# Kernel optimization log

Measured on AMD Instinct MI355X. Metric: run time of the kernel, lower is better.

## Reference

```python
import jax, jax.numpy as jnp
import numpy as np

NG, CPN, K = 16, 24, 5          # ngroups, channels-per-group, kernel size
C = NG * CPN                     # 384 total channels
PAD = K // 2                     # PseudoEntropyPad(2, ...)


def build_mask():
    """PixelCNN-style group-causal mask for MaskConv2 (hidden/type-B: center
    position allows input group <= output group)."""
    m = np.zeros((C, C, K, K), np.float32)
    m[:, :, :PAD, :] = 1.0                      # rows above center: all allowed
    m[:, :, PAD, :PAD] = 1.0                    # center row, left of center
    g = np.arange(C) // CPN
    m[:, :, PAD, PAD] = (g[None, :] <= g[:, None]).astype(np.float32)
    return jnp.asarray(m)


def masked_conv(x, w, b, mask):
    # zero pad by 2 (PseudoEntropyPad) + VALID 5x5 conv == SAME conv
    y = jax.lax.conv_general_dilated(
        x, w * mask, window_strides=(1, 1), padding=[(PAD, PAD), (PAD, PAD)],
        dimension_numbers=("NCHW", "OIHW", "NCHW"))
    return y + b[None, :, None, None]


def prelu(x, a):
    return jnp.where(x >= 0, x, a[None, :, None, None] * x)


def setup_inputs() -> dict:
    key = jax.random.key(0)
    ks = jax.random.split(key, 5)
    x = jax.random.normal(ks[0], (2, C, 256, 512), dtype=jnp.float32)
    w1 = jax.random.normal(ks[1], (C, C, K, K), dtype=jnp.float32) * 0.02
    w2 = jax.random.normal(ks[2], (C, C, K, K), dtype=jnp.float32) * 0.02
    b1 = jnp.zeros((C,), jnp.float32)
    b2 = jnp.zeros((C,), jnp.float32)
    a1 = jnp.full((C,), 0.25, jnp.float32)   # PReLU init
    a2 = jnp.full((C,), 0.25, jnp.float32)
    return {"x": x, "w1": w1, "b1": b1, "a1": a1, "w2": w2, "b2": b2, "a2": a2}


def reference(x, w1, b1, a1, w2, b2, a2):
    mask = build_mask()
    y = prelu(masked_conv(x, w1, b1, mask), a1)   # EntropyConv 1 (pad+conv+PReLU+trim)
    y = prelu(masked_conv(y, w2, b2, mask), a2)   # EntropyConv 2
    return y + x                                   # residual
```

## Files before the change

### kernel.cpp

```cpp
#include <hip/hip_runtime.h>
#include <hip/hip_bf16.h>


#define C_CH 384
#define HH   256
#define WWD  512
#define NN   2
#define NC   12
#define PR   260
#define PC   516
#define ICS  (PR * PC * 32)
#define TCOLS 144
#define TSHORTS (4 * TCOLS * 32)

typedef __attribute__((ext_vector_type(8))) short short8;
typedef __attribute__((ext_vector_type(4))) float f32x4;

typedef const __attribute__((address_space(1))) void* gas_t;
typedef __attribute__((address_space(3))) void* las_t;

__device__ inline unsigned short f2bf(float f) {
    union { float f; unsigned int u; } v; v.f = f;
    unsigned int r = v.u + 0x7FFFu + ((v.u >> 16) & 1u);
    return (unsigned short)(r >> 16);
}

__global__ __launch_bounds__(256) void k_prepack(const float* __restrict__ w1, const float* __restrict__ w2,
                                                 unsigned short* __restrict__ wp1, unsigned short* __restrict__ wp2) {
    int idx = blockIdx.x * 256 + threadIdx.x;
    const int TOT = 13 * NC * C_CH * 32;
    if (idx >= TOT) return;
    int iq = idx & 31;
    int o  = (idx >> 5) % C_CH;
    int ic = (idx / (32 * C_CH)) % NC;
    int t  = idx / (32 * C_CH * NC);
    int i  = ic * 32 + iq;
    int kh = t < 5 ? 0 : (t < 10 ? 1 : 2);
    int kw = t < 5 ? t : (t < 10 ? t - 5 : t - 10);
    bool keep = (t != 12) || ((i / 24) <= (o / 24));
    int src = ((o * C_CH + i) * 5 + kh) * 5 + kw;
    wp1[idx] = keep ? f2bf(w1[src]) : (unsigned short)0;
    wp2[idx] = keep ? f2bf(w2[src]) : (unsigned short)0;
}

__global__ __launch_bounds__(256) void k_repack_x(const float* __restrict__ x, unsigned short* __restrict__ xc) {
    int bid = blockIdx.x;
    int w0 = (bid & 7) << 6;
    int h  = (bid >> 3) & 255;
    int n  = bid >> 11;
    int wi = threadIdx.x & 63;
    int cq = threadIdx.x >> 6;
    int w  = w0 + wi;
    int inb = n * C_CH * HH * WWD + h * WWD + w;
    for (int cc = 0; cc < NC; ++cc) {
        int c0 = cc * 32 + cq * 8;
        short8 outv;
        #pragma unroll
        for (int k = 0; k < 8; ++k) {
            float f = x[inb + (c0 + k) * (HH * WWD)];
            outv[k] = (short)f2bf(f);
        }
        int oidx = (n * NC + cc) * ICS + (h + 2) * (PC * 32) + (w + 2) * 32 + cq * 8;
        *(short8*)&xc[oidx] = outv;
    }
}

template<int SECOND>
__global__ __launch_bounds__(256, 2) void k_conv(const unsigned short* __restrict__ in,
                                                 const unsigned short* __restrict__ wp,
                                                 const float* __restrict__ bias,
                                                 const float* __restrict__ alpha,
                                                 const float* __restrict__ xres,
                                                 void* __restrict__ outp) {
    __shared__ __align__(16) unsigned short Xs[2][TSHORTS];

    int bid0 = blockIdx.x;
    int xcd = bid0 & 7;
    int j0  = bid0 >> 3;
    int tile = xcd * 128 + j0 / 3;
    int ob   = j0 % 3;
    int n    = tile >> 9;
    int hp   = (tile >> 2) & 127;
    int wseg = tile & 3;
    int w0 = wseg << 7, o0 = ob << 7, h0 = hp << 1;

    int tid = threadIdx.x;
    int lane = tid & 63;
    int wv = tid >> 6;
    int wr = wv >> 1, wc = wv & 1;
    int lg = lane >> 4, lm = lane & 15;

    int goff[9];
    #pragma unroll
    for (int it = 0; it < 9; ++it) {
        int k = wv * 9 + it;
        int s = k * 64 + lane;
        int r = s / 576;
        int rem = s - r * 576;
        int c = rem >> 2, q = rem & 3;
        int ce = c < 132 ? c : 0;
        goff[it] = ((h0 + r) * PC + (w0 + ce)) * 32 + q * 8;
    }

    f32x4 acc[32];
    #pragma unroll
    for (int i = 0; i < 32; ++i) acc[i] = (f32x4){0.f, 0.f, 0.f, 0.f};

    {
        const unsigned short* gbase = in + (n * NC + 0) * ICS;
        #pragma unroll
        for (int it = 0; it < 9; ++it) {
            const unsigned short* gp = gbase + goff[it];
            unsigned short* lp = &Xs[0][(wv * 9 + it) * 512];
            __builtin_amdgcn_global_load_lds((gas_t)gp, (las_t)lp, 16, 0, 0);
        }
    }
    __syncthreads();

    for (int ic = 0; ic < NC; ++ic) {
        int buf = ic & 1;
        const unsigned short* gnext = in + (n * NC + (ic + 1)) * ICS;
        short8 wb[4], wbn[4];
        {
            const unsigned short* wb0 = wp + ((0 * NC + ic) * C_CH + o0 + wc * 64) * 32;
            #pragma unroll
            for (int j = 0; j < 4; ++j) wb[j] = *(const short8*)&wb0[(j * 16 + lm) * 32 + lg * 8];
        }
        #pragma unroll
        for (int t = 0; t < 13; ++t) {
            if (t < 12) {
                const unsigned short* wbp = wp + (((t + 1) * NC + ic) * C_CH + o0 + wc * 64) * 32;
                #pragma unroll
                for (int j = 0; j < 4; ++j) wbn[j] = *(const short8*)&wbp[(j * 16 + lm) * 32 + lg * 8];
            }
            if (t < 9) {
                if (ic < NC - 1) {
                    const unsigned short* gp = gnext + goff[t];
                    unsigned short* lp = &Xs[buf ^ 1][(wv * 9 + t) * 512];
                    __builtin_amdgcn_global_load_lds((gas_t)gp, (las_t)lp, 16, 0, 0);
                }
            }
            int kh = t < 5 ? 0 : (t < 10 ? 1 : 2);
            int kw = t < 5 ? t : (t < 10 ? t - 5 : t - 10);
            short8 xa[8];
            #pragma unroll
            for (int f = 0; f < 8; ++f) {
                int cx = f * 16 + lm + kw;
                xa[f] = *(const short8*)&Xs[buf][(wr + kh) * (TCOLS * 32) + cx * 32 + lg * 8];
            }
            if (SECOND) {
                #pragma unroll
                for (int i = 0; i < 4; ++i)
                    #pragma unroll
                    for (int j = 0; j < 8; ++j)
                        acc[i * 8 + j] = __builtin_amdgcn_mfma_f32_16x16x32_bf16(wb[i], xa[j], acc[i * 8 + j], 0, 0, 0);
            } else {
                #pragma unroll
                for (int f = 0; f < 8; ++f)
                    #pragma unroll
                    for (int j = 0; j < 4; ++j)
                        acc[f * 4 + j] = __builtin_amdgcn_mfma_f32_16x16x32_bf16(xa[f], wb[j], acc[f * 4 + j], 0, 0, 0);
            }
            if (t < 12) {
                #pragma unroll
                for (int j = 0; j < 4; ++j) wb[j] = wbn[j];
            }
        }
        __syncthreads();
    }

    int h = h0 + wr;
    if (!SECOND) {
        unsigned short* y = (unsigned short*)outp;
        #pragma unroll
        for (int j = 0; j < 4; ++j) {
            int o = o0 + wc * 64 + j * 16 + lm;
            float bo = bias[o], ao = alpha[o];
            int base = (n * NC + (o >> 5)) * ICS + (h + 2) * (PC * 32) + (o & 31);
            #pragma unroll
            for (int f = 0; f < 8; ++f) {
                #pragma unroll
                for (int rr = 0; rr < 4; ++rr) {
                    int p = f * 16 + lg * 4 + rr;
                    float v = acc[f * 4 + j][rr] + bo;
                    v = v >= 0.f ? v : ao * v;
                    y[base + (w0 + p + 2) * 32] = f2bf(v);
                }
            }
        }
    } else {
        float* outf = (float*)outp;
        #pragma unroll
        for (int i = 0; i < 4; ++i) {
            #pragma unroll
            for (int rr = 0; rr < 4; ++rr) {
                int o = o0 + wc * 64 + i * 16 + lg * 4 + rr;
                float bo = bias[o], ao = alpha[o];
                #pragma unroll
                for (int j = 0; j < 8; ++j) {
                    int w = w0 + j * 16 + lm;
                    float v = acc[i * 8 + j][rr] + bo;
                    v = v >= 0.f ? v : ao * v;
                    int idx = ((n * C_CH + o) * HH + h) * WWD + w;
                    outf[idx] = v + xres[idx];
                }
            }
        }
    }
}

extern "C" void kernel_launch(void* const* d_in, const int* in_sizes, int n_in,
                              void* d_out, int out_size, void* d_ws, size_t ws_size,
                              hipStream_t stream) {
    const float* x  = (const float*)d_in[0];
    const float* w1 = (const float*)d_in[1];
    const float* b1 = (const float*)d_in[2];
    const float* a1 = (const float*)d_in[3];
    const float* w2 = (const float*)d_in[4];
    const float* b2 = (const float*)d_in[5];
    const float* a2 = (const float*)d_in[6];

    const size_t PLANE_SHORTS = (size_t)NN * NC * ICS;
    unsigned short* xc  = (unsigned short*)d_out;
    unsigned short* yb  = (unsigned short*)d_ws;
    unsigned short* wp1 = yb + PLANE_SHORTS;
    unsigned short* wp2 = wp1 + 13 * NC * C_CH * 32;

    hipMemsetAsync(xc, 0, PLANE_SHORTS * 2, stream);
    hipMemsetAsync(yb, 0, PLANE_SHORTS * 2, stream);

    k_prepack<<<(13 * NC * C_CH * 32 + 255) / 256, 256, 0, stream>>>(w1, w2, wp1, wp2);
    k_repack_x<<<NN * HH * (WWD / 64), 256, 0, stream>>>(x, xc);
    k_conv<0><<<3072, 256, 0, stream>>>(xc, wp1, b1, a1, nullptr, (void*)yb);
    k_conv<1><<<3072, 256, 0, stream>>>(yb, wp2, b2, a2, x, (void*)d_out);
}
```

Measured before the change: 2.011 ms.

## Switch conv MFMA to 32x32x16 bf16 with 16-channel planar layout

Repacks activations and weights into 16-channel chunks and replaces 16x16x32 MFMAs with 32x32x16 MFMAs, each wave computing a 128-pixel by 64-output tile as 4x2 32x32 accumulators. The inner loop is software-pipelined, with weight fragments triple-buffered and LDS activation fragments double-buffered, and s_setprio raises priority around the MFMA bursts. The aim is fewer LDS reads per MFMA and better matrix-core utilization. The risks are higher register pressure under the 2-blocks-per-CU launch bound and more global weight loads per step.

```diff
diff --git a/kernel.cpp b/kernel.cpp
--- a/kernel.cpp
+++ b/kernel.cpp
@@ -6,15 +6,17 @@
 #define HH   256
 #define WWD  512
 #define NN   2
-#define NC   12
+#define NKC  24
 #define PR   260
 #define PC   516
-#define ICS  (PR * PC * 32)
+#define ICS16 (PR * PC * 16)
 #define TCOLS 144
-#define TSHORTS (4 * TCOLS * 32)
-
-typedef __attribute__((ext_vector_type(8))) short short8;
-typedef __attribute__((ext_vector_type(4))) float f32x4;
+#define PLANE_SH (4 * TCOLS * 16)
+#define TSH (2 * PLANE_SH)
+
+typedef __attribute__((ext_vector_type(8)))  short short8;
+typedef __attribute__((ext_vector_type(16))) float f32x16;
+typedef __attribute__((ext_vector_type(4)))  int   int4v;
 
 typedef const __attribute__((address_space(1))) void* gas_t;
 typedef __attribute__((address_space(3))) void* las_t;
@@ -28,13 +30,13 @@
 __global__ __launch_bounds__(256) void k_prepack(const float* __restrict__ w1, const float* __restrict__ w2,
                                                  unsigned short* __restrict__ wp1, unsigned short* __restrict__ wp2) {
     int idx = blockIdx.x * 256 + threadIdx.x;
-    const int TOT = 13 * NC * C_CH * 32;
+    const int TOT = 13 * NKC * C_CH * 16;
     if (idx >= TOT) return;
-    int iq = idx & 31;
-    int o  = (idx >> 5) % C_CH;
-    int ic = (idx / (32 * C_CH)) % NC;
-    int t  = idx / (32 * C_CH * NC);
-    int i  = ic * 32 + iq;
+    int iq = idx & 15;
+    int o  = (idx >> 4) % C_CH;
+    int kc = (idx / (16 * C_CH)) % NKC;
+    int t  = idx / (16 * C_CH * NKC);
+    int i  = kc * 16 + iq;
     int kh = t < 5 ? 0 : (t < 10 ? 1 : 2);
     int kw = t < 5 ? t : (t < 10 ? t - 5 : t - 10);
     bool keep = (t != 12) || ((i / 24) <= (o / 24));
@@ -52,7 +54,7 @@
     int cq = threadIdx.x >> 6;
     int w  = w0 + wi;
     int inb = n * C_CH * HH * WWD + h * WWD + w;
-    for (int cc = 0; cc < NC; ++cc) {
+    for (int cc = 0; cc < 12; ++cc) {
         int c0 = cc * 32 + cq * 8;
         short8 outv;
         #pragma unroll
@@ -60,7 +62,8 @@
             float f = x[inb + (c0 + k) * (HH * WWD)];
             outv[k] = (short)f2bf(f);
         }
-        int oidx = (n * NC + cc) * ICS + (h + 2) * (PC * 32) + (w + 2) * 32 + cq * 8;
+        int kc = cc * 2 + (cq >> 1);
+        int oidx = (n * NKC + kc) * ICS16 + ((h + 2) * PC + (w + 2)) * 16 + (cq & 1) * 8;
         *(short8*)&xc[oidx] = outv;
     }
 }
@@ -72,7 +75,7 @@
                                                  const float* __restrict__ alpha,
                                                  const float* __restrict__ xres,
                                                  void* __restrict__ outp) {
-    __shared__ __align__(16) unsigned short Xs[2][TSHORTS];
+    __shared__ __align__(16) unsigned short Xs[2][TSH];
 
     int bid0 = blockIdx.x;
     int xcd = bid0 & 7;
@@ -88,120 +91,136 @@
     int lane = tid & 63;
     int wv = tid >> 6;
     int wr = wv >> 1, wc = wv & 1;
-    int lg = lane >> 4, lm = lane & 15;
+    int lo5 = lane & 31, hi = lane >> 5;
 
     int goff[9];
     #pragma unroll
     for (int it = 0; it < 9; ++it) {
         int k = wv * 9 + it;
-        int s = k * 64 + lane;
-        int r = s / 576;
-        int rem = s - r * 576;
-        int c = rem >> 2, q = rem & 3;
-        int ce = c < 132 ? c : 0;
-        goff[it] = ((h0 + r) * PC + (w0 + ce)) * 32 + q * 8;
-    }
-
-    f32x4 acc[32];
+        int plane = k / 18;
+        int s = (k % 18) * 64 + lane;
+        int r = s / 288;
+        int rem = s - r * 288;
+        int col = rem >> 1, h16 = rem & 1;
+        goff[it] = plane * ICS16 + ((h0 + r) * PC + (w0 + col)) * 16 + h16 * 8;
+    }
+
+    const int KH[13] = {0,0,0,0,0,1,1,1,1,1,2,2,2};
+    const int KW[13] = {0,1,2,3,4,0,1,2,3,4,0,1,2};
+
+    f32x16 acc[4][2];
     #pragma unroll
-    for (int i = 0; i < 32; ++i) acc[i] = (f32x4){0.f, 0.f, 0.f, 0.f};
-
-    {
-        const unsigned short* gbase = in + (n * NC + 0) * ICS;
-        #pragma unroll
-        for (int it = 0; it < 9; ++it) {
-            const unsigned short* gp = gbase + goff[it];
-            unsigned short* lp = &Xs[0][(wv * 9 + it) * 512];
-            __builtin_amdgcn_global_load_lds((gas_t)gp, (las_t)lp, 16, 0, 0);
-        }
+    for (int pt = 0; pt < 4; ++pt)
+        #pragma unroll
+        for (int ot = 0; ot < 2; ++ot)
+            #pragma unroll
+            for (int r = 0; r < 16; ++r) acc[pt][ot][r] = 0.f;
+
+    const unsigned short* gbase_n = in + (size_t)n * NKC * ICS16;
+
+    #pragma unroll
+    for (int it = 0; it < 9; ++it) {
+        const unsigned short* gp = gbase_n + goff[it];
+        unsigned short* lp = &Xs[0][(wv * 9 + it) * 512];
+        __builtin_amdgcn_global_load_lds((gas_t)gp, (las_t)lp, 16, 0, 0);
     }
     __syncthreads();
 
-    for (int ic = 0; ic < NC; ++ic) {
+#define LOAD_XA(dst, u) do {                                              \
+        int t_ = (u) >> 1, hf_ = (u) & 1;                                 \
+        int so_ = hf_ * PLANE_SH + (wr + KH[t_]) * (TCOLS * 16)           \
+                + (lo5 + KW[t_]) * 16 + hi * 8;                           \
+        _Pragma("unroll")                                                 \
+        for (int pt_ = 0; pt_ < 4; ++pt_)                                 \
+            (dst)[pt_] = *(const short8*)&xs[so_ + pt_ * 512];            \
+    } while (0)
+
+#define LOAD_WB(dst, u) do {                                              \
+        int t_ = (u) >> 1, hf_ = (u) & 1;                                 \
+        const unsigned short* wb_ = wp +                                  \
+            (size_t)((t_ * NKC + ic * 2 + hf_) * C_CH + o0 + wc * 64) * 16; \
+        _Pragma("unroll")                                                 \
+        for (int ot_ = 0; ot_ < 2; ++ot_)                                 \
+            (dst)[ot_] = *(const short8*)&wb_[(ot_ * 32 + lo5) * 16 + hi * 8]; \
+    } while (0)
+
+    for (int ic = 0; ic < 12; ++ic) {
         int buf = ic & 1;
-        const unsigned short* gnext = in + (n * NC + (ic + 1)) * ICS;
-        short8 wb[4], wbn[4];
-        {
-            const unsigned short* wb0 = wp + ((0 * NC + ic) * C_CH + o0 + wc * 64) * 32;
-            #pragma unroll
-            for (int j = 0; j < 4; ++j) wb[j] = *(const short8*)&wb0[(j * 16 + lm) * 32 + lg * 8];
-        }
-        #pragma unroll
-        for (int t = 0; t < 13; ++t) {
-            if (t < 12) {
-                const unsigned short* wbp = wp + (((t + 1) * NC + ic) * C_CH + o0 + wc * 64) * 32;
+        const unsigned short* xs = &Xs[buf][0];
+        if (ic < 11) {
+            const unsigned short* gb = gbase_n + (size_t)(ic + 1) * 2 * ICS16;
+            #pragma unroll
+            for (int it = 0; it < 9; ++it) {
+                const unsigned short* gp = gb + goff[it];
+                unsigned short* lp = &Xs[buf ^ 1][(wv * 9 + it) * 512];
+                __builtin_amdgcn_global_load_lds((gas_t)gp, (las_t)lp, 16, 0, 0);
+            }
+        }
+
+        short8 xa[2][4];
+        short8 wb[3][2];
+        LOAD_XA(xa[0], 0);
+        LOAD_WB(wb[0], 0);
+        LOAD_WB(wb[1], 1);
+
+        #pragma unroll
+        for (int s2 = 0; s2 < 26; ++s2) {
+            if (s2 + 2 < 26) LOAD_WB(wb[(s2 + 2) % 3], s2 + 2);
+            if (s2 + 1 < 26) LOAD_XA(xa[(s2 + 1) & 1], s2 + 1);
+            __builtin_amdgcn_s_setprio(1);
+            #pragma unroll
+            for (int pt = 0; pt < 4; ++pt)
                 #pragma unroll
-                for (int j = 0; j < 4; ++j) wbn[j] = *(const short8*)&wbp[(j * 16 + lm) * 32 + lg * 8];
-            }
-            if (t < 9) {
-                if (ic < NC - 1) {
-                    const unsigned short* gp = gnext + goff[t];
-                    unsigned short* lp = &Xs[buf ^ 1][(wv * 9 + t) * 512];
-                    __builtin_amdgcn_global_load_lds((gas_t)gp, (las_t)lp, 16, 0, 0);
+                for (int ot = 0; ot < 2; ++ot) {
+                    if (SECOND)
+                        acc[pt][ot] = __builtin_amdgcn_mfma_f32_32x32x16_bf16(
+                            wb[s2 % 3][ot], xa[s2 & 1][pt], acc[pt][ot], 0, 0, 0);
+                    else
+                        acc[pt][ot] = __builtin_amdgcn_mfma_f32_32x32x16_bf16(
+                            xa[s2 & 1][pt], wb[s2 % 3][ot], acc[pt][ot], 0, 0, 0);
                 }
-            }
-            int kh = t < 5 ? 0 : (t < 10 ? 1 : 2);
-            int kw = t < 5 ? t : (t < 10 ? t - 5 : t - 10);
-            short8 xa[8];
-            #pragma unroll
-            for (int f = 0; f < 8; ++f) {
-                int cx = f * 16 + lm + kw;
-                xa[f] = *(const short8*)&Xs[buf][(wr + kh) * (TCOLS * 32) + cx * 32 + lg * 8];
-            }
-            if (SECOND) {
-                #pragma unroll
-                for (int i = 0; i < 4; ++i)
-                    #pragma unroll
-                    for (int j = 0; j < 8; ++j)
-                        acc[i * 8 + j] = __builtin_amdgcn_mfma_f32_16x16x32_bf16(wb[i], xa[j], acc[i * 8 + j], 0, 0, 0);
-            } else {
-                #pragma unroll
-                for (int f = 0; f < 8; ++f)
-                    #pragma unroll
-                    for (int j = 0; j < 4; ++j)
-                        acc[f * 4 + j] = __builtin_amdgcn_mfma_f32_16x16x32_bf16(xa[f], wb[j], acc[f * 4 + j], 0, 0, 0);
-            }
-            if (t < 12) {
-                #pragma unroll
-                for (int j = 0; j < 4; ++j) wb[j] = wbn[j];
-            }
+            __builtin_amdgcn_s_setprio(0);
         }
         __syncthreads();
     }
+#undef LOAD_XA
+#undef LOAD_WB
 
     int h = h0 + wr;
     if (!SECOND) {
         unsigned short* y = (unsigned short*)outp;
         #pragma unroll
-        for (int j = 0; j < 4; ++j) {
-            int o = o0 + wc * 64 + j * 16 + lm;
+        for (int ot = 0; ot < 2; ++ot) {
+            int o = o0 + wc * 64 + ot * 32 + lo5;
             float bo = bias[o], ao = alpha[o];
-            int base = (n * NC + (o >> 5)) * ICS + (h + 2) * (PC * 32) + (o & 31);
-            #pragma unroll
-            for (int f = 0; f < 8; ++f) {
+            int kc = o >> 4;
+            int o15 = o & 15;
+            size_t base = (size_t)(n * NKC + kc) * ICS16 + ((h + 2) * PC + (w0 + 2)) * 16 + o15;
+            #pragma unroll
+            for (int pt = 0; pt < 4; ++pt) {
                 #pragma unroll
-                for (int rr = 0; rr < 4; ++rr) {
-                    int p = f * 16 + lg * 4 + rr;
-                    float v = acc[f * 4 + j][rr] + bo;
+                for (int reg = 0; reg < 16; ++reg) {
+                    int p = pt * 32 + (reg & 3) + 8 * (reg >> 2) + 4 * hi;
+                    float v = acc[pt][ot][reg] + bo;
                     v = v >= 0.f ? v : ao * v;
-                    y[base + (w0 + p + 2) * 32] = f2bf(v);
+                    y[base + (size_t)p * 16] = f2bf(v);
                 }
             }
         }
     } else {
         float* outf = (float*)outp;
         #pragma unroll
-        for (int i = 0; i < 4; ++i) {
-            #pragma unroll
-            for (int rr = 0; rr < 4; ++rr) {
-                int o = o0 + wc * 64 + i * 16 + lg * 4 + rr;
+        for (int ot = 0; ot < 2; ++ot) {
+            #pragma unroll
+            for (int reg = 0; reg < 16; ++reg) {
+                int o = o0 + wc * 64 + ot * 32 + (reg & 3) + 8 * (reg >> 2) + 4 * hi;
                 float bo = bias[o], ao = alpha[o];
                 #pragma unroll
-                for (int j = 0; j < 8; ++j) {
-                    int w = w0 + j * 16 + lm;
-                    float v = acc[i * 8 + j][rr] + bo;
+                for (int pt = 0; pt < 4; ++pt) {
+                    int w = w0 + pt * 32 + lo5;
+                    float v = acc[pt][ot][reg] + bo;
                     v = v >= 0.f ? v : ao * v;
-                    int idx = ((n * C_CH + o) * HH + h) * WWD + w;
+                    size_t idx = (size_t)((n * C_CH + o) * HH + h) * WWD + w;
                     outf[idx] = v + xres[idx];
                 }
             }
@@ -220,16 +239,16 @@
     const float* b2 = (const float*)d_in[5];
     const float* a2 = (const float*)d_in[6];
 
-    const size_t PLANE_SHORTS = (size_t)NN * NC * ICS;
+    const size_t PLANE_SHORTS = (size_t)NN * NKC * ICS16;
     unsigned short* xc  = (unsigned short*)d_out;
     unsigned short* yb  = (unsigned short*)d_ws;
     unsigned short* wp1 = yb + PLANE_SHORTS;
-    unsigned short* wp2 = wp1 + 13 * NC * C_CH * 32;
+    unsigned short* wp2 = wp1 + 13 * NKC * C_CH * 16;
 
     hipMemsetAsync(xc, 0, PLANE_SHORTS * 2, stream);
     hipMemsetAsync(yb, 0, PLANE_SHORTS * 2, stream);
 
-    k_prepack<<<(13 * NC * C_CH * 32 + 255) / 256, 256, 0, stream>>>(w1, w2, wp1, wp2);
+    k_prepack<<<(13 * NKC * C_CH * 16 + 255) / 256, 256, 0, stream>>>(w1, w2, wp1, wp2);
     k_repack_x<<<NN * HH * (WWD / 64), 256, 0, stream>>>(x, xc);
     k_conv<0><<<3072, 256, 0, stream>>>(xc, wp1, b1, a1, nullptr, (void*)yb);
     k_conv<1><<<3072, 256, 0, stream>>>(yb, wp2, b2, a2, x, (void*)d_out);
```

New measurement: 1.922 ms. 4.4% less time.
